# Performance work log

Measured on AMD Instinct MI355X. Metric: run time of the kernel, lower is better.

Reference implementation:

```python
import jax, jax.numpy as jnp
import numpy as np

N = 4096
DIN = 512
H = 128    # hidden_dim per head
K = 4      # num_heads
DOUT = 16  # output classes
ALPHA = 0.2  # leaky relu negative slope


def setup_inputs() -> dict:
    key = jax.random.key(0)
    ks = jax.random.split(key, 8)
    X = jax.random.normal(ks[0], (N, DIN), jnp.float32)
    # sparse random graph (p=0.01), non-zero where edges exist
    adj = (jax.random.uniform(ks[1], (N, N)) < 0.01).astype(jnp.float32)
    W1 = jax.random.normal(ks[2], (K, DIN, H), jnp.float32) * np.float32(1.0 / np.sqrt(DIN))
    a_src1 = jax.random.normal(ks[3], (K, H), jnp.float32) * np.float32(0.1)
    a_dst1 = jax.random.normal(ks[4], (K, H), jnp.float32) * np.float32(0.1)
    W2 = jax.random.normal(ks[5], (K * H, DOUT), jnp.float32) * np.float32(1.0 / np.sqrt(K * H))
    a_src2 = jax.random.normal(ks[6], (DOUT,), jnp.float32) * np.float32(0.1)
    a_dst2 = jax.random.normal(ks[7], (DOUT,), jnp.float32) * np.float32(0.1)
    return {"X": X, "adj": adj, "W1": W1, "a_src1": a_src1, "a_dst1": a_dst1,
            "W2": W2, "a_src2": a_src2, "a_dst2": a_dst2}


def gat_multihead(h, mask, W, a_src, a_dst):
    # h: (N, Din), W: (K, Din, O), a_src/a_dst: (K, O), mask: (N, N) bool
    Wh = jnp.einsum('ni,kio->kno', h, W)                      # (K, N, O)
    src = jnp.einsum('kno,ko->kn', Wh, a_src)                 # (K, N)
    dst = jnp.einsum('kno,ko->kn', Wh, a_dst)                 # (K, N)
    e = jax.nn.leaky_relu(src[:, :, None] + dst[:, None, :], ALPHA)  # (K, N, N)
    e = jnp.where(mask[None], e, -jnp.inf)
    attn = jax.nn.softmax(e, axis=-1)                         # rows sum to 1 (self-loop guarantees >=1 edge)
    return jnp.einsum('knm,kmo->kno', attn, Wh)               # (K, N, O)


def reference(X, adj, W1, a_src1, a_dst1, W2, a_src2, a_dst2):
    # mask = (adj + I) > 0
    mask = (adj + jnp.eye(N, dtype=adj.dtype)) > 0
    # layer 1: 4 heads, concatenated, then ELU (eval mode: no dropout)
    h1 = gat_multihead(X, mask, W1, a_src1, a_dst1)           # (K, N, H)
    h1 = jnp.transpose(h1, (1, 0, 2)).reshape(N, K * H)       # concat heads -> (N, K*H)
    h1 = jax.nn.elu(h1)
    # layer 2: single head, mean over heads == the head itself
    h2 = gat_multihead(h1, mask, W2[None], a_src2[None], a_dst2[None])[0]  # (N, DOUT)
    return jax.nn.log_softmax(h2, axis=1)
```

## Files before the change

kernel.cpp:

```cpp
#include <hip/hip_runtime.h>
#include <hip/hip_bf16.h>


typedef __attribute__((ext_vector_type(4))) float floatx4;
typedef __attribute__((ext_vector_type(8))) short short8;
typedef __attribute__((ext_vector_type(4))) unsigned short ushortx4;
typedef __attribute__((ext_vector_type(4))) unsigned int uintx4;
typedef unsigned short u16b;

#define GN 4096
#define LDP 40

__device__ __forceinline__ u16b f2bf(float f) {
  union { float f; unsigned int i; } v; v.f = f;
  unsigned int r = v.i + 0x7FFF + ((v.i >> 16) & 1);
  return (u16b)(r >> 16);
}
__device__ __forceinline__ float bflo(unsigned u) {
  union { unsigned i; float f; } v; v.i = u << 16; return v.f;
}
__device__ __forceinline__ float bfhi(unsigned u) {
  union { unsigned i; float f; } v; v.i = u & 0xffff0000u; return v.f;
}

__global__ __launch_bounds__(512) void k_fused1(const float* __restrict__ adj,
    const float* __restrict__ X, const float* __restrict__ W1,
    const float* __restrict__ as1, const float* __restrict__ ad1,
    u16b* __restrict__ mask, u16b* __restrict__ Wh1bf,
    float* __restrict__ src1t, float* __restrict__ dst1t) {
  int b = blockIdx.x, t = threadIdx.x;
  int lane = t & 63, w = t >> 6;
  if (b >= 256) {
    int n = (b - 256) * 2 + (t >> 8);
    int cg = t & 255;
    const float* ap = adj + (size_t)n * 4096 + cg * 16;
    floatx4 v0 = *(const floatx4*)(ap);
    floatx4 v1 = *(const floatx4*)(ap + 4);
    floatx4 v2 = *(const floatx4*)(ap + 8);
    floatx4 v3 = *(const floatx4*)(ap + 12);
    unsigned bits = 0;
#pragma unroll
    for (int i = 0; i < 4; ++i) {
      bits |= (unsigned)(v0[i] != 0.f) << i;
      bits |= (unsigned)(v1[i] != 0.f) << (4 + i);
      bits |= (unsigned)(v2[i] != 0.f) << (8 + i);
      bits |= (unsigned)(v3[i] != 0.f) << (12 + i);
    }
    if ((n >> 4) == cg) bits |= 1u << (n & 15);
    mask[(size_t)n * 256 + cg] = (u16b)bits;
  } else {
    __shared__ u16b Ab[64 * LDP];
    __shared__ u16b Bb[128 * LDP];
    __shared__ float sps[4][64], sds[4][64];
    int p = ((b >> 5) << 3) | (b & 7);
    int hd = (b >> 3) & 3;
    int rb = p * 64;
    const float* Wk = W1 + (size_t)hd * 65536;
    int wr = w >> 2, wc = w & 3, lh = lane >> 4, lm = lane & 15;
    int ar = t >> 2, aq = t & 3;
    int u = t - 256, kk0 = (u & 7) * 4, c0 = (u >> 3) * 4;
    floatx4 pa0, pa1, pb0, pb1, pb2, pb3;
    if (t < 256) {
      const float* ap = X + (size_t)(rb + ar) * 512 + aq * 8;
      pa0 = *(const floatx4*)(ap);
      pa1 = *(const floatx4*)(ap + 4);
    } else {
      const float* bp = Wk + (size_t)kk0 * 128 + c0;
      pb0 = *(const floatx4*)(bp);
      pb1 = *(const floatx4*)(bp + 128);
      pb2 = *(const floatx4*)(bp + 256);
      pb3 = *(const floatx4*)(bp + 384);
    }
    floatx4 acc[2][2] = {};
    for (int kk = 0; kk < 512; kk += 32) {
      if (t < 256) {
        short8 a;
        a[0] = (short)f2bf(pa0[0]); a[1] = (short)f2bf(pa0[1]);
        a[2] = (short)f2bf(pa0[2]); a[3] = (short)f2bf(pa0[3]);
        a[4] = (short)f2bf(pa1[0]); a[5] = (short)f2bf(pa1[1]);
        a[6] = (short)f2bf(pa1[2]); a[7] = (short)f2bf(pa1[3]);
        *(short8*)(&Ab[ar * LDP + aq * 8]) = a;
      } else {
#pragma unroll
        for (int cq = 0; cq < 4; ++cq) {
          ushortx4 v;
          v[0] = f2bf(pb0[cq]); v[1] = f2bf(pb1[cq]);
          v[2] = f2bf(pb2[cq]); v[3] = f2bf(pb3[cq]);
          *(ushortx4*)(&Bb[(c0 + cq) * LDP + kk0]) = v;
        }
      }
      __syncthreads();
      if (kk + 32 < 512) {
        if (t < 256) {
          const float* ap = X + (size_t)(rb + ar) * 512 + kk + 32 + aq * 8;
          pa0 = *(const floatx4*)(ap);
          pa1 = *(const floatx4*)(ap + 4);
        } else {
          const float* bp = Wk + (size_t)(kk + 32 + kk0) * 128 + c0;
          pb0 = *(const floatx4*)(bp);
          pb1 = *(const floatx4*)(bp + 128);
          pb2 = *(const floatx4*)(bp + 256);
          pb3 = *(const floatx4*)(bp + 384);
        }
      }
      short8 a0 = *(const short8*)(&Ab[(wr * 32      + lm) * LDP + lh * 8]);
      short8 a1 = *(const short8*)(&Ab[(wr * 32 + 16 + lm) * LDP + lh * 8]);
      short8 b0 = *(const short8*)(&Bb[(wc * 32      + lm) * LDP + lh * 8]);
      short8 b1 = *(const short8*)(&Bb[(wc * 32 + 16 + lm) * LDP + lh * 8]);
      acc[0][0] = __builtin_amdgcn_mfma_f32_16x16x32_bf16(a0, b0, acc[0][0], 0, 0, 0);
      acc[0][1] = __builtin_amdgcn_mfma_f32_16x16x32_bf16(a0, b1, acc[0][1], 0, 0, 0);
      acc[1][0] = __builtin_amdgcn_mfma_f32_16x16x32_bf16(a1, b0, acc[1][0], 0, 0, 0);
      acc[1][1] = __builtin_amdgcn_mfma_f32_16x16x32_bf16(a1, b1, acc[1][1], 0, 0, 0);
      __syncthreads();
    }
#pragma unroll
    for (int m = 0; m < 2; ++m)
#pragma unroll
      for (int n2 = 0; n2 < 2; ++n2)
#pragma unroll
        for (int j = 0; j < 4; ++j)
          Wh1bf[(size_t)(rb + wr * 32 + m * 16 + lh * 4 + j) * 512
                + hd * 128 + wc * 32 + n2 * 16 + lm] = f2bf(acc[m][n2][j]);
    float asv[2], adv[2];
#pragma unroll
    for (int n2 = 0; n2 < 2; ++n2) {
      asv[n2] = as1[hd * 128 + wc * 32 + n2 * 16 + lm];
      adv[n2] = ad1[hd * 128 + wc * 32 + n2 * 16 + lm];
    }
#pragma unroll
    for (int m = 0; m < 2; ++m)
#pragma unroll
      for (int j = 0; j < 4; ++j) {
        float ps = acc[m][0][j] * asv[0] + acc[m][1][j] * asv[1];
        float pd = acc[m][0][j] * adv[0] + acc[m][1][j] * adv[1];
#pragma unroll
        for (int off = 8; off >= 1; off >>= 1) {
          ps += __shfl_xor(ps, off, 16);
          pd += __shfl_xor(pd, off, 16);
        }
        if (lm == 0) {
          sps[wc][wr * 32 + m * 16 + lh * 4 + j] = ps;
          sds[wc][wr * 32 + m * 16 + lh * 4 + j] = pd;
        }
      }
    __syncthreads();
    if (t < 64) {
      src1t[(size_t)(rb + t) * 4 + hd] = sps[0][t] + sps[1][t] + sps[2][t] + sps[3][t];
      dst1t[(size_t)(rb + t) * 4 + hd] = sds[0][t] + sds[1][t] + sds[2][t] + sds[3][t];
    }
  }
}

__global__ __launch_bounds__(256) void k_attn1(const u16b* __restrict__ mask,
    const u16b* __restrict__ Wh1bf,
    const float* __restrict__ src1t, const float* __restrict__ dst1t,
    const float* __restrict__ W2, const float* __restrict__ as2,
    const float* __restrict__ ad2, float* __restrict__ Wh2,
    float* __restrict__ src2, float* __restrict__ dst2) {
  int n = blockIdx.x, t = threadIdx.x, lane = t & 63, w = t >> 6;
  __shared__ u16b lst[512];
  __shared__ int2 pr[4][512];
  __shared__ float h1row[512];
  __shared__ float redw[4][16];
  __shared__ int wtot[4];
  unsigned M = mask[(size_t)n * 256 + t];
  int pc = __popc(M);
  int incl = pc;
#pragma unroll
  for (int off = 1; off <= 32; off <<= 1) {
    int v = __shfl_up(incl, off);
    if (lane >= off) incl += v;
  }
  if (lane == 63) wtot[w] = incl;
  float snw = src1t[n * 4 + w];
  __syncthreads();
  int base = 0;
  for (int w2 = 0; w2 < w; ++w2) base += wtot[w2];
  int cnt = wtot[0] + wtot[1] + wtot[2] + wtot[3];
  int pos = base + incl - pc;
  while (M) {
    int c = __builtin_ctz(M);
    lst[pos++] = (u16b)(t * 16 + c);
    M &= M - 1;
  }
  __syncthreads();
  float ee[8];
  int mo[8];
  float mx = -1e30f, sm = 0.f;
#pragma unroll
  for (int rep = 0; rep < 8; ++rep) {
    int li = lane + rep * 64;
    if (li < cnt) {
      int m = lst[li];
      float e = snw + dst1t[m * 4 + w];
      e = e > 0.f ? e : 0.2f * e;
      ee[rep] = e; mo[rep] = m << 10;
      if (e > mx) { sm = sm * __expf(mx - e) + 1.f; mx = e; }
      else sm += __expf(e - mx);
    }
  }
#pragma unroll
  for (int off = 32; off >= 1; off >>= 1) {
    float mm = __shfl_xor(mx, off);
    float so = __shfl_xor(sm, off);
    float Mx = fmaxf(mx, mm);
    sm = sm * __expf(mx - Mx) + so * __expf(mm - Mx);
    mx = Mx;
  }
  float R = 1.f / sm;
#pragma unroll
  for (int rep = 0; rep < 8; ++rep) {
    int li = lane + rep * 64;
    if (li < cnt) {
      int2 pv;
      pv.x = mo[rep];
      pv.y = __float_as_int(__expf(ee[rep] - mx) * R);
      pr[w][li] = pv;
    }
  }
  __syncthreads();
  int q = lane >> 4, p = lane & 15;
  const char* gbase = (const char*)Wh1bf + 256 * w + 16 * p;
  float a[8] = {0.f, 0.f, 0.f, 0.f, 0.f, 0.f, 0.f, 0.f};
  for (int li = q; li < cnt; li += 4) {
    int2 pw = pr[w][li];
    float wv = __int_as_float(pw.y);
    uintx4 u = *(const uintx4*)(gbase + pw.x);
    a[0] = fmaf(wv, bflo(u[0]), a[0]); a[1] = fmaf(wv, bfhi(u[0]), a[1]);
    a[2] = fmaf(wv, bflo(u[1]), a[2]); a[3] = fmaf(wv, bfhi(u[1]), a[3]);
    a[4] = fmaf(wv, bflo(u[2]), a[4]); a[5] = fmaf(wv, bfhi(u[2]), a[5]);
    a[6] = fmaf(wv, bflo(u[3]), a[6]); a[7] = fmaf(wv, bfhi(u[3]), a[7]);
  }
#pragma unroll
  for (int j = 0; j < 8; ++j) {
    a[j] += __shfl_xor(a[j], 16);
    a[j] += __shfl_xor(a[j], 32);
  }
  if (q == 0) {
#pragma unroll
    for (int j = 0; j < 8; ++j) {
      float v = a[j];
      v = v > 0.f ? v : __expf(v) - 1.f;
      h1row[128 * w + 8 * p + j] = v;
    }
  }
  __syncthreads();
  {
    int o = lane & 15, ig = lane >> 4;
    float accw = 0.f;
    for (int i = w * 128 + ig; i < (w + 1) * 128; i += 4)
      accw = fmaf(h1row[i], W2[i * 16 + o], accw);
    accw += __shfl_xor(accw, 16);
    accw += __shfl_xor(accw, 32);
    if (lane < 16) redw[w][o] = accw;
  }
  __syncthreads();
  if (t < 16) {
    float v = redw[0][t] + redw[1][t] + redw[2][t] + redw[3][t];
    Wh2[n * 16 + t] = v;
    float ps = v * as2[t];
    float pd = v * ad2[t];
#pragma unroll
    for (int off = 8; off >= 1; off >>= 1) {
      ps += __shfl_xor(ps, off, 16);
      pd += __shfl_xor(pd, off, 16);
    }
    if (t == 0) { src2[n] = ps; dst2[n] = pd; }
  }
}

__global__ __launch_bounds__(256) void k_attn2(const u16b* __restrict__ mask,
    const float* __restrict__ Wh2, const float* __restrict__ src2,
    const float* __restrict__ dst2, float* __restrict__ out) {
  int w = threadIdx.x >> 6, lane = threadIdx.x & 63;
  int n = blockIdx.x * 4 + w;
  __shared__ int2 pr4[4][512];
  int2* pr = pr4[w];
  float snv = src2[n];
  unsigned long long B = *(const unsigned long long*)((const char*)mask + (size_t)n * 512 + lane * 8);
  int pc = __popcll(B);
  int incl = pc;
#pragma unroll
  for (int off = 1; off <= 32; off <<= 1) {
    int v = __shfl_up(incl, off);
    if (lane >= off) incl += v;
  }
  int cnt = __shfl(incl, 63);
  int pos = incl - pc;
  float mx = -1e30f, sm = 0.f;
  while (B) {
    int c = __builtin_ctzll(B);
    int m = lane * 64 + c;
    float e = snv + dst2[m];
    e = e > 0.f ? e : 0.2f * e;
    if (e > mx) { sm = sm * __expf(mx - e) + 1.f; mx = e; }
    else sm += __expf(e - mx);
    int2 pv; pv.x = m << 4; pv.y = __float_as_int(e);
    pr[pos++] = pv;
    B &= B - 1;
  }
#pragma unroll
  for (int off = 32; off >= 1; off >>= 1) {
    float mo = __shfl_xor(mx, off);
    float so = __shfl_xor(sm, off);
    float M = fmaxf(mx, mo);
    sm = sm * __expf(mx - M) + so * __expf(mo - M);
    mx = M;
  }
  float R = 1.f / sm;
  int o = lane & 15, g = lane >> 4;
  float acc = 0.f;
  for (int li = g; li < cnt; li += 4) {
    int2 pv = pr[li];
    float wgt = __expf(__int_as_float(pv.y) - mx) * R;
    acc = fmaf(wgt, Wh2[pv.x + o], acc);
  }
  acc += __shfl_xor(acc, 16);
  acc += __shfl_xor(acc, 32);
  float vm = acc;
#pragma unroll
  for (int off = 8; off >= 1; off >>= 1) vm = fmaxf(vm, __shfl_xor(vm, off, 16));
  float ex = __expf(acc - vm);
#pragma unroll
  for (int off = 8; off >= 1; off >>= 1) ex += __shfl_xor(ex, off, 16);
  if (lane < 16) out[(size_t)n * 16 + lane] = acc - vm - __logf(ex);
}

extern "C" void kernel_launch(void* const* d_in, const int* in_sizes, int n_in,
                              void* d_out, int out_size, void* d_ws, size_t ws_size,
                              hipStream_t stream) {
  const float* X   = (const float*)d_in[0];
  const float* adj = (const float*)d_in[1];
  const float* W1  = (const float*)d_in[2];
  const float* as1 = (const float*)d_in[3];
  const float* ad1 = (const float*)d_in[4];
  const float* W2  = (const float*)d_in[5];
  const float* as2 = (const float*)d_in[6];
  const float* ad2 = (const float*)d_in[7];
  float* out = (float*)d_out;

  char* ws = (char*)d_ws;
  float* src1t = (float*)ws;
  float* dst1t = (float*)(ws + (64 << 10));
  float* src2  = (float*)(ws + (128 << 10));
  float* dst2  = (float*)(ws + (144 << 10));
  float* Wh2   = (float*)(ws + (160 << 10));
  u16b*  mask  = (u16b*)(ws + (512 << 10));
  u16b*  Wh1bf = (u16b*)(ws + (4ull << 20));

  k_fused1<<<dim3(2304), dim3(512), 0, stream>>>(adj, X, W1, as1, ad1,
                                                 mask, Wh1bf, src1t, dst1t);
  k_attn1<<<dim3(GN), dim3(256), 0, stream>>>(mask, Wh1bf, src1t, dst1t,
                                              W2, as2, ad2, Wh2, src2, dst2);
  k_attn2<<<dim3(1024), dim3(256), 0, stream>>>(mask, Wh2, src2, dst2, out);
}
```

Before: 67.45 us.

## Split mask/GEMM kernels and process one node per wavefront in layer-1 attention

The fused mask+GEMM kernel is split into two separate launches. The layer-1 attention kernel is restructured so each wavefront handles one node across all four heads, with no block-level syncs. Attention weights are stored as fp16 in shared memory, and each lane gathers its 8-wide slice of the full 512-column Wh1 row. This removes the __syncthreads barriers and makes the neighbor gather wider and more coalesced. In exchange it adds an extra kernel launch, serializes the mask build with the GEMM, and gives up some precision in the fp16 weights.

```diff
diff --git a/kernel.cpp b/kernel.cpp
--- a/kernel.cpp
+++ b/kernel.cpp
@@ -1,5 +1,6 @@
 #include <hip/hip_runtime.h>
 #include <hip/hip_bf16.h>
+#include <hip/hip_fp16.h>
 
 
 typedef __attribute__((ext_vector_type(4))) float floatx4;
@@ -23,131 +24,132 @@
   union { unsigned i; float f; } v; v.i = u & 0xffff0000u; return v.f;
 }
 
-__global__ __launch_bounds__(512) void k_fused1(const float* __restrict__ adj,
-    const float* __restrict__ X, const float* __restrict__ W1,
-    const float* __restrict__ as1, const float* __restrict__ ad1,
-    u16b* __restrict__ mask, u16b* __restrict__ Wh1bf,
+__global__ __launch_bounds__(512) void k_mask(const float* __restrict__ adj,
+                                              u16b* __restrict__ mask) {
+  int t = threadIdx.x;
+  int n = blockIdx.x * 2 + (t >> 8);
+  int cg = t & 255;
+  const float* ap = adj + (size_t)n * 4096 + cg * 16;
+  floatx4 v0 = *(const floatx4*)(ap);
+  floatx4 v1 = *(const floatx4*)(ap + 4);
+  floatx4 v2 = *(const floatx4*)(ap + 8);
+  floatx4 v3 = *(const floatx4*)(ap + 12);
+  unsigned bits = 0;
+#pragma unroll
+  for (int i = 0; i < 4; ++i) {
+    bits |= (unsigned)(v0[i] != 0.f) << i;
+    bits |= (unsigned)(v1[i] != 0.f) << (4 + i);
+    bits |= (unsigned)(v2[i] != 0.f) << (8 + i);
+    bits |= (unsigned)(v3[i] != 0.f) << (12 + i);
+  }
+  if ((n >> 4) == cg) bits |= 1u << (n & 15);
+  mask[(size_t)n * 256 + cg] = (u16b)bits;
+}
+
+__global__ __launch_bounds__(512) void k_gemm1(const float* __restrict__ X,
+    const float* __restrict__ W1, const float* __restrict__ as1,
+    const float* __restrict__ ad1, u16b* __restrict__ Wh1bf,
     float* __restrict__ src1t, float* __restrict__ dst1t) {
   int b = blockIdx.x, t = threadIdx.x;
   int lane = t & 63, w = t >> 6;
-  if (b >= 256) {
-    int n = (b - 256) * 2 + (t >> 8);
-    int cg = t & 255;
-    const float* ap = adj + (size_t)n * 4096 + cg * 16;
-    floatx4 v0 = *(const floatx4*)(ap);
-    floatx4 v1 = *(const floatx4*)(ap + 4);
-    floatx4 v2 = *(const floatx4*)(ap + 8);
-    floatx4 v3 = *(const floatx4*)(ap + 12);
-    unsigned bits = 0;
-#pragma unroll
-    for (int i = 0; i < 4; ++i) {
-      bits |= (unsigned)(v0[i] != 0.f) << i;
-      bits |= (unsigned)(v1[i] != 0.f) << (4 + i);
-      bits |= (unsigned)(v2[i] != 0.f) << (8 + i);
-      bits |= (unsigned)(v3[i] != 0.f) << (12 + i);
-    }
-    if ((n >> 4) == cg) bits |= 1u << (n & 15);
-    mask[(size_t)n * 256 + cg] = (u16b)bits;
+  __shared__ u16b Ab[64 * LDP];
+  __shared__ u16b Bb[128 * LDP];
+  __shared__ float sps[4][64], sds[4][64];
+  int p = ((b >> 5) << 3) | (b & 7);
+  int hd = (b >> 3) & 3;
+  int rb = p * 64;
+  const float* Wk = W1 + (size_t)hd * 65536;
+  int wr = w >> 2, wc = w & 3, lh = lane >> 4, lm = lane & 15;
+  int ar = t >> 2, aq = t & 3;
+  int u = t - 256, kk0 = (u & 7) * 4, c0 = (u >> 3) * 4;
+  floatx4 pa0, pa1, pb0, pb1, pb2, pb3;
+  if (t < 256) {
+    const float* ap = X + (size_t)(rb + ar) * 512 + aq * 8;
+    pa0 = *(const floatx4*)(ap);
+    pa1 = *(const floatx4*)(ap + 4);
   } else {
-    __shared__ u16b Ab[64 * LDP];
-    __shared__ u16b Bb[128 * LDP];
-    __shared__ float sps[4][64], sds[4][64];
-    int p = ((b >> 5) << 3) | (b & 7);
-    int hd = (b >> 3) & 3;
-    int rb = p * 64;
-    const float* Wk = W1 + (size_t)hd * 65536;
-    int wr = w >> 2, wc = w & 3, lh = lane >> 4, lm = lane & 15;
-    int ar = t >> 2, aq = t & 3;
-    int u = t - 256, kk0 = (u & 7) * 4, c0 = (u >> 3) * 4;
-    floatx4 pa0, pa1, pb0, pb1, pb2, pb3;
+    const float* bp = Wk + (size_t)kk0 * 128 + c0;
+    pb0 = *(const floatx4*)(bp);
+    pb1 = *(const floatx4*)(bp + 128);
+    pb2 = *(const floatx4*)(bp + 256);
+    pb3 = *(const floatx4*)(bp + 384);
+  }
+  floatx4 acc[2][2] = {};
+  for (int kk = 0; kk < 512; kk += 32) {
     if (t < 256) {
-      const float* ap = X + (size_t)(rb + ar) * 512 + aq * 8;
-      pa0 = *(const floatx4*)(ap);
-      pa1 = *(const floatx4*)(ap + 4);
+      short8 a;
+      a[0] = (short)f2bf(pa0[0]); a[1] = (short)f2bf(pa0[1]);
+      a[2] = (short)f2bf(pa0[2]); a[3] = (short)f2bf(pa0[3]);
+      a[4] = (short)f2bf(pa1[0]); a[5] = (short)f2bf(pa1[1]);
+      a[6] = (short)f2bf(pa1[2]); a[7] = (short)f2bf(pa1[3]);
+      *(short8*)(&Ab[ar * LDP + aq * 8]) = a;
     } else {
-      const float* bp = Wk + (size_t)kk0 * 128 + c0;
-      pb0 = *(const floatx4*)(bp);
-      pb1 = *(const floatx4*)(bp + 128);
-      pb2 = *(const floatx4*)(bp + 256);
-      pb3 = *(const floatx4*)(bp + 384);
-    }
-    floatx4 acc[2][2] = {};
-    for (int kk = 0; kk < 512; kk += 32) {
+#pragma unroll
+      for (int cq = 0; cq < 4; ++cq) {
+        ushortx4 v;
+        v[0] = f2bf(pb0[cq]); v[1] = f2bf(pb1[cq]);
+        v[2] = f2bf(pb2[cq]); v[3] = f2bf(pb3[cq]);
+        *(ushortx4*)(&Bb[(c0 + cq) * LDP + kk0]) = v;
+      }
+    }
+    __syncthreads();
+    if (kk + 32 < 512) {
       if (t < 256) {
-        short8 a;
-        a[0] = (short)f2bf(pa0[0]); a[1] = (short)f2bf(pa0[1]);
-        a[2] = (short)f2bf(pa0[2]); a[3] = (short)f2bf(pa0[3]);
-        a[4] = (short)f2bf(pa1[0]); a[5] = (short)f2bf(pa1[1]);
-        a[6] = (short)f2bf(pa1[2]); a[7] = (short)f2bf(pa1[3]);
-        *(short8*)(&Ab[ar * LDP + aq * 8]) = a;
+        const float* ap = X + (size_t)(rb + ar) * 512 + kk + 32 + aq * 8;
+        pa0 = *(const floatx4*)(ap);
+        pa1 = *(const floatx4*)(ap + 4);
       } else {
-#pragma unroll
-        for (int cq = 0; cq < 4; ++cq) {
-          ushortx4 v;
-          v[0] = f2bf(pb0[cq]); v[1] = f2bf(pb1[cq]);
-          v[2] = f2bf(pb2[cq]); v[3] = f2bf(pb3[cq]);
-          *(ushortx4*)(&Bb[(c0 + cq) * LDP + kk0]) = v;
-        }
+        const float* bp = Wk + (size_t)(kk + 32 + kk0) * 128 + c0;
+        pb0 = *(const floatx4*)(bp);
+        pb1 = *(const floatx4*)(bp + 128);
+        pb2 = *(const floatx4*)(bp + 256);
+        pb3 = *(const floatx4*)(bp + 384);
       }
-      __syncthreads();
-      if (kk + 32 < 512) {
-        if (t < 256) {
-          const float* ap = X + (size_t)(rb + ar) * 512 + kk + 32 + aq * 8;
-          pa0 = *(const floatx4*)(ap);
-          pa1 = *(const floatx4*)(ap + 4);
-        } else {
-          const float* bp = Wk + (size_t)(kk + 32 + kk0) * 128 + c0;
-          pb0 = *(const floatx4*)(bp);
-          pb1 = *(const floatx4*)(bp + 128);
-          pb2 = *(const floatx4*)(bp + 256);
-          pb3 = *(const floatx4*)(bp + 384);
-        }
+    }
+    short8 a0 = *(const short8*)(&Ab[(wr * 32      + lm) * LDP + lh * 8]);
+    short8 a1 = *(const short8*)(&Ab[(wr * 32 + 16 + lm) * LDP + lh * 8]);
+    short8 b0 = *(const short8*)(&Bb[(wc * 32      + lm) * LDP + lh * 8]);
+    short8 b1 = *(const short8*)(&Bb[(wc * 32 + 16 + lm) * LDP + lh * 8]);
+    acc[0][0] = __builtin_amdgcn_mfma_f32_16x16x32_bf16(a0, b0, acc[0][0], 0, 0, 0);
+    acc[0][1] = __builtin_amdgcn_mfma_f32_16x16x32_bf16(a0, b1, acc[0][1], 0, 0, 0);
+    acc[1][0] = __builtin_amdgcn_mfma_f32_16x16x32_bf16(a1, b0, acc[1][0], 0, 0, 0);
+    acc[1][1] = __builtin_amdgcn_mfma_f32_16x16x32_bf16(a1, b1, acc[1][1], 0, 0, 0);
+    __syncthreads();
+  }
+#pragma unroll
+  for (int m = 0; m < 2; ++m)
+#pragma unroll
+    for (int n2 = 0; n2 < 2; ++n2)
+#pragma unroll
+      for (int j = 0; j < 4; ++j)
+        Wh1bf[(size_t)(rb + wr * 32 + m * 16 + lh * 4 + j) * 512
+              + hd * 128 + wc * 32 + n2 * 16 + lm] = f2bf(acc[m][n2][j]);
+  float asv[2], adv[2];
+#pragma unroll
+  for (int n2 = 0; n2 < 2; ++n2) {
+    asv[n2] = as1[hd * 128 + wc * 32 + n2 * 16 + lm];
+    adv[n2] = ad1[hd * 128 + wc * 32 + n2 * 16 + lm];
+  }
+#pragma unroll
+  for (int m = 0; m < 2; ++m)
+#pragma unroll
+    for (int j = 0; j < 4; ++j) {
+      float ps = acc[m][0][j] * asv[0] + acc[m][1][j] * asv[1];
+      float pd = acc[m][0][j] * adv[0] + acc[m][1][j] * adv[1];
+#pragma unroll
+      for (int off = 8; off >= 1; off >>= 1) {
+        ps += __shfl_xor(ps, off, 16);
+        pd += __shfl_xor(pd, off, 16);
       }
-      short8 a0 = *(const short8*)(&Ab[(wr * 32      + lm) * LDP + lh * 8]);
-      short8 a1 = *(const short8*)(&Ab[(wr * 32 + 16 + lm) * LDP + lh * 8]);
-      short8 b0 = *(const short8*)(&Bb[(wc * 32      + lm) * LDP + lh * 8]);
-      short8 b1 = *(const short8*)(&Bb[(wc * 32 + 16 + lm) * LDP + lh * 8]);
-      acc[0][0] = __builtin_amdgcn_mfma_f32_16x16x32_bf16(a0, b0, acc[0][0], 0, 0, 0);
-      acc[0][1] = __builtin_amdgcn_mfma_f32_16x16x32_bf16(a0, b1, acc[0][1], 0, 0, 0);
-      acc[1][0] = __builtin_amdgcn_mfma_f32_16x16x32_bf16(a1, b0, acc[1][0], 0, 0, 0);
-      acc[1][1] = __builtin_amdgcn_mfma_f32_16x16x32_bf16(a1, b1, acc[1][1], 0, 0, 0);
-      __syncthreads();
-    }
-#pragma unroll
-    for (int m = 0; m < 2; ++m)
-#pragma unroll
-      for (int n2 = 0; n2 < 2; ++n2)
-#pragma unroll
-        for (int j = 0; j < 4; ++j)
-          Wh1bf[(size_t)(rb + wr * 32 + m * 16 + lh * 4 + j) * 512
-                + hd * 128 + wc * 32 + n2 * 16 + lm] = f2bf(acc[m][n2][j]);
-    float asv[2], adv[2];
-#pragma unroll
-    for (int n2 = 0; n2 < 2; ++n2) {
-      asv[n2] = as1[hd * 128 + wc * 32 + n2 * 16 + lm];
-      adv[n2] = ad1[hd * 128 + wc * 32 + n2 * 16 + lm];
-    }
-#pragma unroll
-    for (int m = 0; m < 2; ++m)
-#pragma unroll
-      for (int j = 0; j < 4; ++j) {
-        float ps = acc[m][0][j] * asv[0] + acc[m][1][j] * asv[1];
-        float pd = acc[m][0][j] * adv[0] + acc[m][1][j] * adv[1];
-#pragma unroll
-        for (int off = 8; off >= 1; off >>= 1) {
-          ps += __shfl_xor(ps, off, 16);
-          pd += __shfl_xor(pd, off, 16);
-        }
-        if (lm == 0) {
-          sps[wc][wr * 32 + m * 16 + lh * 4 + j] = ps;
-          sds[wc][wr * 32 + m * 16 + lh * 4 + j] = pd;
-        }
+      if (lm == 0) {
+        sps[wc][wr * 32 + m * 16 + lh * 4 + j] = ps;
+        sds[wc][wr * 32 + m * 16 + lh * 4 + j] = pd;
       }
-    __syncthreads();
-    if (t < 64) {
-      src1t[(size_t)(rb + t) * 4 + hd] = sps[0][t] + sps[1][t] + sps[2][t] + sps[3][t];
-      dst1t[(size_t)(rb + t) * 4 + hd] = sds[0][t] + sds[1][t] + sds[2][t] + sds[3][t];
-    }
+    }
+  __syncthreads();
+  if (t < 64) {
+    src1t[(size_t)(rb + t) * 4 + hd] = sps[0][t] + sps[1][t] + sps[2][t] + sps[3][t];
+    dst1t[(size_t)(rb + t) * 4 + hd] = sds[0][t] + sds[1][t] + sds[2][t] + sds[3][t];
   }
 }
 
@@ -157,75 +159,76 @@
     const float* __restrict__ W2, const float* __restrict__ as2,
     const float* __restrict__ ad2, float* __restrict__ Wh2,
     float* __restrict__ src2, float* __restrict__ dst2) {
-  int n = blockIdx.x, t = threadIdx.x, lane = t & 63, w = t >> 6;
-  __shared__ u16b lst[512];
-  __shared__ int2 pr[4][512];
-  __shared__ float h1row[512];
-  __shared__ float redw[4][16];
-  __shared__ int wtot[4];
-  unsigned M = mask[(size_t)n * 256 + t];
-  int pc = __popc(M);
+  int w = threadIdx.x >> 6, lane = threadIdx.x & 63;
+  int n = blockIdx.x * 4 + w;
+  __shared__ u16b lst4[4][512];
+  __shared__ unsigned short ewh4[4][2048];
+  __shared__ float h1w4[4][512];
+  u16b* lst = lst4[w];
+  unsigned short* ewh = ewh4[w];
+  float* h1w = h1w4[w];
+  unsigned long long B = *(const unsigned long long*)((const char*)mask + (size_t)n * 512 + lane * 8);
+  int pc = __popcll(B);
   int incl = pc;
 #pragma unroll
   for (int off = 1; off <= 32; off <<= 1) {
     int v = __shfl_up(incl, off);
     if (lane >= off) incl += v;
   }
-  if (lane == 63) wtot[w] = incl;
-  float snw = src1t[n * 4 + w];
-  __syncthreads();
-  int base = 0;
-  for (int w2 = 0; w2 < w; ++w2) base += wtot[w2];
-  int cnt = wtot[0] + wtot[1] + wtot[2] + wtot[3];
-  int pos = base + incl - pc;
-  while (M) {
-    int c = __builtin_ctz(M);
-    lst[pos++] = (u16b)(t * 16 + c);
-    M &= M - 1;
-  }
-  __syncthreads();
-  float ee[8];
-  int mo[8];
-  float mx = -1e30f, sm = 0.f;
-#pragma unroll
-  for (int rep = 0; rep < 8; ++rep) {
-    int li = lane + rep * 64;
-    if (li < cnt) {
-      int m = lst[li];
-      float e = snw + dst1t[m * 4 + w];
+  int cnt = __shfl(incl, 63);
+  int pos = incl - pc;
+  while (B) {
+    int c = __builtin_ctzll(B);
+    lst[pos++] = (u16b)(lane * 64 + c);
+    B &= B - 1;
+  }
+  floatx4 sn = *(const floatx4*)(src1t + (size_t)n * 4);
+  float mx[4], sm[4];
+#pragma unroll
+  for (int k = 0; k < 4; ++k) { mx[k] = -1e30f; sm[k] = 0.f; }
+  for (int li = lane; li < cnt; li += 64) {
+    int m = lst[li];
+    floatx4 dv = *(const floatx4*)(dst1t + (size_t)m * 4);
+    ushortx4 ev;
+#pragma unroll
+    for (int k = 0; k < 4; ++k) {
+      float e = sn[k] + dv[k];
       e = e > 0.f ? e : 0.2f * e;
-      ee[rep] = e; mo[rep] = m << 10;
-      if (e > mx) { sm = sm * __expf(mx - e) + 1.f; mx = e; }
-      else sm += __expf(e - mx);
-    }
-  }
-#pragma unroll
-  for (int off = 32; off >= 1; off >>= 1) {
-    float mm = __shfl_xor(mx, off);
-    float so = __shfl_xor(sm, off);
-    float Mx = fmaxf(mx, mm);
-    sm = sm * __expf(mx - Mx) + so * __expf(mm - Mx);
-    mx = Mx;
-  }
-  float R = 1.f / sm;
-#pragma unroll
-  for (int rep = 0; rep < 8; ++rep) {
-    int li = lane + rep * 64;
-    if (li < cnt) {
-      int2 pv;
-      pv.x = mo[rep];
-      pv.y = __float_as_int(__expf(ee[rep] - mx) * R);
-      pr[w][li] = pv;
-    }
-  }
-  __syncthreads();
-  int q = lane >> 4, p = lane & 15;
-  const char* gbase = (const char*)Wh1bf + 256 * w + 16 * p;
+      ev[k] = __half_as_ushort(__float2half(e));
+      if (e > mx[k]) { sm[k] = sm[k] * __expf(mx[k] - e) + 1.f; mx[k] = e; }
+      else sm[k] += __expf(e - mx[k]);
+    }
+    *(ushortx4*)(&ewh[li * 4]) = ev;
+  }
+#pragma unroll
+  for (int k = 0; k < 4; ++k) {
+#pragma unroll
+    for (int off = 32; off >= 1; off >>= 1) {
+      float mo = __shfl_xor(mx[k], off);
+      float so = __shfl_xor(sm[k], off);
+      float M = fmaxf(mx[k], mo);
+      sm[k] = sm[k] * __expf(mx[k] - M) + so * __expf(mo - M);
+      mx[k] = M;
+    }
+    sm[k] = 1.f / sm[k];
+  }
+  for (int li = lane; li < cnt; li += 64) {
+    ushortx4 ev = *(const ushortx4*)(&ewh[li * 4]);
+#pragma unroll
+    for (int k = 0; k < 4; ++k) {
+      float e = __half2float(__ushort_as_half(ev[k]));
+      ev[k] = __half_as_ushort(__float2half(__expf(e - mx[k]) * sm[k]));
+    }
+    *(ushortx4*)(&ewh[li * 4]) = ev;
+  }
+  int hd = lane >> 4;
+  const char* gb = (const char*)Wh1bf + lane * 16;
   float a[8] = {0.f, 0.f, 0.f, 0.f, 0.f, 0.f, 0.f, 0.f};
-  for (int li = q; li < cnt; li += 4) {
-    int2 pw = pr[w][li];
-    float wv = __int_as_float(pw.y);
-    uintx4 u = *(const uintx4*)(gbase + pw.x);
+#pragma unroll 2
+  for (int li = 0; li < cnt; ++li) {
+    int m = lst[li];
+    float wv = __half2float(__ushort_as_half(ewh[li * 4 + hd]));
+    uintx4 u = *(const uintx4*)(gb + (size_t)m * 1024);
     a[0] = fmaf(wv, bflo(u[0]), a[0]); a[1] = fmaf(wv, bfhi(u[0]), a[1]);
     a[2] = fmaf(wv, bflo(u[1]), a[2]); a[3] = fmaf(wv, bfhi(u[1]), a[3]);
     a[4] = fmaf(wv, bflo(u[2]), a[4]); a[5] = fmaf(wv, bfhi(u[2]), a[5]);
@@ -233,39 +236,31 @@
   }
 #pragma unroll
   for (int j = 0; j < 8; ++j) {
-    a[j] += __shfl_xor(a[j], 16);
-    a[j] += __shfl_xor(a[j], 32);
-  }
-  if (q == 0) {
-#pragma unroll
-    for (int j = 0; j < 8; ++j) {
-      float v = a[j];
-      v = v > 0.f ? v : __expf(v) - 1.f;
-      h1row[128 * w + 8 * p + j] = v;
-    }
-  }
-  __syncthreads();
-  {
-    int o = lane & 15, ig = lane >> 4;
-    float accw = 0.f;
-    for (int i = w * 128 + ig; i < (w + 1) * 128; i += 4)
-      accw = fmaf(h1row[i], W2[i * 16 + o], accw);
-    accw += __shfl_xor(accw, 16);
-    accw += __shfl_xor(accw, 32);
-    if (lane < 16) redw[w][o] = accw;
-  }
-  __syncthreads();
-  if (t < 16) {
-    float v = redw[0][t] + redw[1][t] + redw[2][t] + redw[3][t];
-    Wh2[n * 16 + t] = v;
-    float ps = v * as2[t];
-    float pd = v * ad2[t];
+    float v = a[j];
+    h1w[lane * 8 + j] = v > 0.f ? v : __expf(v) - 1.f;
+  }
+  int o = lane & 15, ig = lane >> 4;
+  float p0 = 0.f, p1 = 0.f, p2 = 0.f, p3 = 0.f;
+  for (int j = 0; j < 128; j += 4) {
+    int i0 = ig + 4 * j;
+    p0 = fmaf(h1w[i0],      W2[i0 * 16 + o],        p0);
+    p1 = fmaf(h1w[i0 + 4],  W2[(i0 + 4) * 16 + o],  p1);
+    p2 = fmaf(h1w[i0 + 8],  W2[(i0 + 8) * 16 + o],  p2);
+    p3 = fmaf(h1w[i0 + 12], W2[(i0 + 12) * 16 + o], p3);
+  }
+  float pacc = (p0 + p1) + (p2 + p3);
+  pacc += __shfl_xor(pacc, 16);
+  pacc += __shfl_xor(pacc, 32);
+  if (lane < 16) {
+    Wh2[(size_t)n * 16 + lane] = pacc;
+    float ps = pacc * as2[lane];
+    float pd = pacc * ad2[lane];
 #pragma unroll
     for (int off = 8; off >= 1; off >>= 1) {
       ps += __shfl_xor(ps, off, 16);
       pd += __shfl_xor(pd, off, 16);
     }
-    if (t == 0) { src2[n] = ps; dst2[n] = pd; }
+    if (lane == 0) { src2[n] = ps; dst2[n] = pd; }
   }
 }
 
@@ -348,9 +343,9 @@
   u16b*  mask  = (u16b*)(ws + (512 << 10));
   u16b*  Wh1bf = (u16b*)(ws + (4ull << 20));
 
-  k_fused1<<<dim3(2304), dim3(512), 0, stream>>>(adj, X, W1, as1, ad1,
-                                                 mask, Wh1bf, src1t, dst1t);
-  k_attn1<<<dim3(GN), dim3(256), 0, stream>>>(mask, Wh1bf, src1t, dst1t,
-                                              W2, as2, ad2, Wh2, src2, dst2);
+  k_mask <<<dim3(2048), dim3(512), 0, stream>>>(adj, mask);
+  k_gemm1<<<dim3(256),  dim3(512), 0, stream>>>(X, W1, as1, ad1, Wh1bf, src1t, dst1t);
+  k_attn1<<<dim3(1024), dim3(256), 0, stream>>>(mask, Wh1bf, src1t, dst1t,
+                                                W2, as2, ad2, Wh2, src2, dst2);
   k_attn2<<<dim3(1024), dim3(256), 0, stream>>>(mask, Wh2, src2, dst2, out);
 }
```

After: 70.52 us. 4.6% more time.

## Restructure GAT layer-1 attention kernel around per-wave scans and chunked gathers

Applied to the files above, without the earlier changes.

Each wave now scans the row's 4096-bit mask itself, using 64-bit words and a wave-level prefix sum. This removes the cross-wave totals and two block barriers, at the price of all four waves redundantly writing the same shared neighbor list. Attention logits and normalized weights are stored as fp16 in shared memory rather than fp32 offset/weight pairs. The neighbor gather now gives each lane two output columns and processes eight neighbors per chunk to increase loads in flight, and the W2 projection loop is unrolled with four accumulators. It also adds an occupancy hint of 8 blocks per CU, and fp16 weights add some rounding error.

```diff
diff --git a/kernel.cpp b/kernel.cpp
--- a/kernel.cpp
+++ b/kernel.cpp
@@ -1,11 +1,11 @@
 #include <hip/hip_runtime.h>
 #include <hip/hip_bf16.h>
+#include <hip/hip_fp16.h>
 
 
 typedef __attribute__((ext_vector_type(4))) float floatx4;
 typedef __attribute__((ext_vector_type(8))) short short8;
 typedef __attribute__((ext_vector_type(4))) unsigned short ushortx4;
-typedef __attribute__((ext_vector_type(4))) unsigned int uintx4;
 typedef unsigned short u16b;
 
 #define GN 4096
@@ -21,6 +21,9 @@
 }
 __device__ __forceinline__ float bfhi(unsigned u) {
   union { unsigned i; float f; } v; v.i = u & 0xffff0000u; return v.f;
+}
+__device__ __forceinline__ float h2f(unsigned short h) {
+  return __half2float(__ushort_as_half(h));
 }
 
 __global__ __launch_bounds__(512) void k_fused1(const float* __restrict__ adj,
@@ -151,113 +154,104 @@
   }
 }
 
-__global__ __launch_bounds__(256) void k_attn1(const u16b* __restrict__ mask,
+__global__ __launch_bounds__(256, 8) void k_attn1(const u16b* __restrict__ mask,
     const u16b* __restrict__ Wh1bf,
     const float* __restrict__ src1t, const float* __restrict__ dst1t,
     const float* __restrict__ W2, const float* __restrict__ as2,
     const float* __restrict__ ad2, float* __restrict__ Wh2,
     float* __restrict__ src2, float* __restrict__ dst2) {
-  int n = blockIdx.x, t = threadIdx.x, lane = t & 63, w = t >> 6;
+  int w = threadIdx.x >> 6, lane = threadIdx.x & 63;
+  int n = blockIdx.x;
   __shared__ u16b lst[512];
-  __shared__ int2 pr[4][512];
+  __shared__ unsigned short ewh[4][512];
   __shared__ float h1row[512];
   __shared__ float redw[4][16];
-  __shared__ int wtot[4];
-  unsigned M = mask[(size_t)n * 256 + t];
-  int pc = __popc(M);
+  unsigned long long B = *(const unsigned long long*)((const char*)mask + (size_t)n * 512 + lane * 8);
+  int pc = __popcll(B);
   int incl = pc;
 #pragma unroll
   for (int off = 1; off <= 32; off <<= 1) {
     int v = __shfl_up(incl, off);
     if (lane >= off) incl += v;
   }
-  if (lane == 63) wtot[w] = incl;
-  float snw = src1t[n * 4 + w];
-  __syncthreads();
-  int base = 0;
-  for (int w2 = 0; w2 < w; ++w2) base += wtot[w2];
-  int cnt = wtot[0] + wtot[1] + wtot[2] + wtot[3];
-  int pos = base + incl - pc;
-  while (M) {
-    int c = __builtin_ctz(M);
-    lst[pos++] = (u16b)(t * 16 + c);
-    M &= M - 1;
-  }
-  __syncthreads();
-  float ee[8];
-  int mo[8];
+  int cnt = __shfl(incl, 63);
+  int pos = incl - pc;
+  while (B) {
+    int c = __builtin_ctzll(B);
+    lst[pos++] = (u16b)(lane * 64 + c);
+    B &= B - 1;
+  }
+  int nch = (cnt + 7) >> 3;
+  for (int i = cnt + lane; i < nch * 8; i += 64) { lst[i] = 0; ewh[w][i] = 0; }
+  float snw = src1t[(size_t)n * 4 + w];
   float mx = -1e30f, sm = 0.f;
-#pragma unroll
-  for (int rep = 0; rep < 8; ++rep) {
-    int li = lane + rep * 64;
-    if (li < cnt) {
-      int m = lst[li];
-      float e = snw + dst1t[m * 4 + w];
-      e = e > 0.f ? e : 0.2f * e;
-      ee[rep] = e; mo[rep] = m << 10;
-      if (e > mx) { sm = sm * __expf(mx - e) + 1.f; mx = e; }
-      else sm += __expf(e - mx);
-    }
+  for (int li = lane; li < cnt; li += 64) {
+    int m = lst[li];
+    float e = snw + dst1t[(size_t)m * 4 + w];
+    e = e > 0.f ? e : 0.2f * e;
+    ewh[w][li] = __half_as_ushort(__float2half(e));
+    if (e > mx) { sm = sm * __expf(mx - e) + 1.f; mx = e; }
+    else sm += __expf(e - mx);
   }
 #pragma unroll
   for (int off = 32; off >= 1; off >>= 1) {
-    float mm = __shfl_xor(mx, off);
+    float mo = __shfl_xor(mx, off);
     float so = __shfl_xor(sm, off);
-    float Mx = fmaxf(mx, mm);
-    sm = sm * __expf(mx - Mx) + so * __expf(mm - Mx);
-    mx = Mx;
+    float M = fmaxf(mx, mo);
+    sm = sm * __expf(mx - M) + so * __expf(mo - M);
+    mx = M;
   }
   float R = 1.f / sm;
-#pragma unroll
-  for (int rep = 0; rep < 8; ++rep) {
-    int li = lane + rep * 64;
-    if (li < cnt) {
-      int2 pv;
-      pv.x = mo[rep];
-      pv.y = __float_as_int(__expf(ee[rep] - mx) * R);
-      pr[w][li] = pv;
-    }
-  }
-  __syncthreads();
-  int q = lane >> 4, p = lane & 15;
-  const char* gbase = (const char*)Wh1bf + 256 * w + 16 * p;
-  float a[8] = {0.f, 0.f, 0.f, 0.f, 0.f, 0.f, 0.f, 0.f};
-  for (int li = q; li < cnt; li += 4) {
-    int2 pw = pr[w][li];
-    float wv = __int_as_float(pw.y);
-    uintx4 u = *(const uintx4*)(gbase + pw.x);
-    a[0] = fmaf(wv, bflo(u[0]), a[0]); a[1] = fmaf(wv, bfhi(u[0]), a[1]);
-    a[2] = fmaf(wv, bflo(u[1]), a[2]); a[3] = fmaf(wv, bfhi(u[1]), a[3]);
-    a[4] = fmaf(wv, bflo(u[2]), a[4]); a[5] = fmaf(wv, bfhi(u[2]), a[5]);
-    a[6] = fmaf(wv, bflo(u[3]), a[6]); a[7] = fmaf(wv, bfhi(u[3]), a[7]);
-  }
-#pragma unroll
-  for (int j = 0; j < 8; ++j) {
-    a[j] += __shfl_xor(a[j], 16);
-    a[j] += __shfl_xor(a[j], 32);
-  }
-  if (q == 0) {
-#pragma unroll
-    for (int j = 0; j < 8; ++j) {
-      float v = a[j];
-      v = v > 0.f ? v : __expf(v) - 1.f;
-      h1row[128 * w + 8 * p + j] = v;
-    }
-  }
+  for (int li = lane; li < cnt; li += 64) {
+    float e = h2f(ewh[w][li]);
+    ewh[w][li] = __half_as_ushort(__float2half(__expf(e - mx) * R));
+  }
+  const char* gb = (const char*)Wh1bf + w * 256 + lane * 4;
+  float a0 = 0.f, a1 = 0.f;
+  for (int c = 0; c < nch; ++c) {
+    int mreg[8]; float wreg[8]; unsigned ureg[8];
+#pragma unroll
+    for (int q = 0; q < 8; ++q) {
+      int li = c * 8 + q;
+      mreg[q] = lst[li];
+      wreg[q] = h2f(ewh[w][li]);
+    }
+#pragma unroll
+    for (int q = 0; q < 8; ++q)
+      ureg[q] = *(const unsigned*)(gb + (size_t)mreg[q] * 1024);
+#pragma unroll
+    for (int q = 0; q < 8; ++q) {
+      a0 = fmaf(wreg[q], bflo(ureg[q]), a0);
+      a1 = fmaf(wreg[q], bfhi(ureg[q]), a1);
+    }
+  }
+  a0 = a0 > 0.f ? a0 : __expf(a0) - 1.f;
+  a1 = a1 > 0.f ? a1 : __expf(a1) - 1.f;
+  h1row[w * 128 + lane * 2]     = a0;
+  h1row[w * 128 + lane * 2 + 1] = a1;
   __syncthreads();
   {
     int o = lane & 15, ig = lane >> 4;
-    float accw = 0.f;
-    for (int i = w * 128 + ig; i < (w + 1) * 128; i += 4)
-      accw = fmaf(h1row[i], W2[i * 16 + o], accw);
-    accw += __shfl_xor(accw, 16);
-    accw += __shfl_xor(accw, 32);
-    if (lane < 16) redw[w][o] = accw;
+    int base = w * 128 + ig;
+    float p0 = 0.f, p1 = 0.f, p2 = 0.f, p3 = 0.f;
+#pragma unroll
+    for (int m = 0; m < 32; m += 4) {
+      int i0 = base + 4 * m;
+      p0 = fmaf(h1row[i0],      W2[i0 * 16 + o],        p0);
+      p1 = fmaf(h1row[i0 + 4],  W2[(i0 + 4) * 16 + o],  p1);
+      p2 = fmaf(h1row[i0 + 8],  W2[(i0 + 8) * 16 + o],  p2);
+      p3 = fmaf(h1row[i0 + 12], W2[(i0 + 12) * 16 + o], p3);
+    }
+    float pacc = (p0 + p1) + (p2 + p3);
+    pacc += __shfl_xor(pacc, 16);
+    pacc += __shfl_xor(pacc, 32);
+    if (lane < 16) redw[w][lane] = pacc;
   }
   __syncthreads();
-  if (t < 16) {
+  if (threadIdx.x < 16) {
+    int t = threadIdx.x;
     float v = redw[0][t] + redw[1][t] + redw[2][t] + redw[3][t];
-    Wh2[n * 16 + t] = v;
+    Wh2[(size_t)n * 16 + t] = v;
     float ps = v * as2[t];
     float pd = v * ad2[t];
 #pragma unroll
```

Result: faster. 55.12 us, median of 3 (-18.3%).
